# Performance work log

Measured on AMD Instinct MI355X. Metric: run time of the kernel, lower is better.

The kernel has to match this reference:

```python
import jax, jax.numpy as jnp
import numpy as np

INPUT_SIZE = 1000
EMB = 1024          # 2**ceil(log2(input_size))
NQ = 10             # log2(EMB)
NL = 3              # n_qlayers (hardcoded in module)
B = 4096


def _rot(phi, theta, omega):
    # PennyLane qml.Rot(phi, theta, omega) = RZ(omega) RY(theta) RZ(phi)
    c = jnp.cos(theta * 0.5).astype(jnp.complex64)
    s = jnp.sin(theta * 0.5).astype(jnp.complex64)
    ea = jnp.exp(-0.5j * (phi + omega))   # e^{-i(phi+omega)/2}
    eb = jnp.exp(0.5j * (phi - omega))    # e^{ i(phi-omega)/2}
    row0 = jnp.stack([ea * c, -eb * s])
    row1 = jnp.stack([jnp.conj(eb) * s, jnp.conj(ea) * c])
    return jnp.stack([row0, row1])        # [2, 2] complex64


def _apply_1q(psi, U, q):
    # psi: [B] + [2]*NQ ; contract qubit axis q+1 with U
    psi = jnp.tensordot(psi, U, axes=[[q + 1], [1]])
    return jnp.moveaxis(psi, -1, q + 1)


def _apply_cnot(psi, c, t):
    c_ax, t_ax = c + 1, t + 1
    psi0 = jax.lax.index_in_dim(psi, 0, axis=c_ax, keepdims=False)
    psi1 = jax.lax.index_in_dim(psi, 1, axis=c_ax, keepdims=False)
    f_ax = t_ax - 1 if t_ax > c_ax else t_ax
    psi1 = jnp.flip(psi1, axis=f_ax)      # X on target when control=1
    return jnp.stack([psi0, psi1], axis=c_ax)


def _circuit(x, w):
    # AmplitudeEmbedding(normalize=True) + StronglyEntanglingLayers + probs
    norm = jnp.sqrt(jnp.sum(x * x, axis=1, keepdims=True))
    psi = (x / norm).astype(jnp.complex64)
    b = psi.shape[0]
    psi = psi.reshape((b,) + (2,) * NQ)   # wire 0 = most-significant bit
    for l in range(NL):
        for q in range(NQ):
            psi = _apply_1q(psi, _rot(w[l, q, 0], w[l, q, 1], w[l, q, 2]), q)
        r = l % (NQ - 1) + 1              # default SEL ranges
        for q in range(NQ):
            psi = _apply_cnot(psi, q, (q + r) % NQ)
    return (psi.real ** 2 + psi.imag ** 2).reshape(b, -1)  # probs [B, 2**NQ]


def setup_inputs() -> dict:
    key = jax.random.key(0)
    ks = jax.random.split(key, 12)
    d = {
        'inputs': jax.random.normal(ks[0], (B, INPUT_SIZE), jnp.float32),
        'weightsEnc': 0.1 * jax.random.normal(ks[1], (NL, NQ, 3), jnp.float32),
        'weightsDec': 0.1 * jax.random.normal(ks[2], (NL, NQ, 3), jnp.float32),
        'W0': jax.random.normal(ks[3], (INPUT_SIZE, EMB), jnp.float32) / np.sqrt(INPUT_SIZE),
        'b0': jnp.zeros((EMB,), jnp.float32),
        'W1': jax.random.normal(ks[4], (EMB, 2 * EMB), jnp.float32) / np.sqrt(EMB),
        'b1': jnp.zeros((2 * EMB,), jnp.float32),
        'W2': jax.random.normal(ks[5], (2 * EMB, EMB), jnp.float32) / np.sqrt(2 * EMB),
        'b2': jnp.zeros((EMB,), jnp.float32),
        'W3': jax.random.normal(ks[6], (EMB, INPUT_SIZE), jnp.float32) / np.sqrt(EMB),
        'b3': jnp.zeros((INPUT_SIZE,), jnp.float32),
    }
    return d


def reference(inputs, weightsEnc, weightsDec, W0, b0, W1, b1, W2, b2, W3, b3):
    x = inputs @ W0 + b0                 # Dense(embedding_dim)
    x = _circuit(x, weightsEnc)          # encoder qnode (vmapped over batch)
    x = x @ W1 + b1                      # Dense(2*embedding_dim)
    x = x @ W2 + b2                      # Dense(embedding_dim)
    x = _circuit(x, weightsDec)          # decoder qnode
    x = x @ W3 + b3                      # Dense(input_size)
    x = jnp.abs(x)
    return x / jnp.sum(x, axis=1, keepdims=True)
```

## Files before the change

kernel.cpp:

```cpp
#include <hip/hip_runtime.h>
#include <math.h>


#define B_SZ 4096
#define EMB 1024
#define NQ 10
#define NL 3

typedef __bf16 bf16x8 __attribute__((ext_vector_type(8)));
typedef float f32x4 __attribute__((ext_vector_type(4)));
typedef unsigned short u16x8 __attribute__((ext_vector_type(8)));

__device__ __forceinline__ unsigned short f2bf_rne(float f) {
    unsigned int u = __float_as_uint(f);
    u += 0x7FFFu + ((u >> 16) & 1u);
    return (unsigned short)(u >> 16);
}
__device__ __forceinline__ float bf2f(unsigned short h) {
    return __uint_as_float(((unsigned int)h) << 16);
}
__device__ __forceinline__ float lane_bcast(float v, int l) {
    return __uint_as_float(__builtin_amdgcn_readlane(__float_as_uint(v), l));
}

template<int M>
__device__ __forceinline__ float lane_xor(float v) {
    if constexpr (M == 1)
        return __uint_as_float(__builtin_amdgcn_mov_dpp(__float_as_uint(v), 0xB1, 0xF, 0xF, true));
    else if constexpr (M == 2)
        return __uint_as_float(__builtin_amdgcn_mov_dpp(__float_as_uint(v), 0x4E, 0xF, 0xF, true));
    else if constexpr (M == 8)
        return __uint_as_float(__builtin_amdgcn_mov_dpp(__float_as_uint(v), 0x128, 0xF, 0xF, true));
    else if constexpr (M == 4)
        return __uint_as_float(__builtin_amdgcn_ds_swizzle(__float_as_uint(v), 0x101F));
    else if constexpr (M == 16)
        return __uint_as_float(__builtin_amdgcn_ds_swizzle(__float_as_uint(v), 0x401F));
    else
        return __shfl_xor(v, 32, 64);
}

__device__ __forceinline__ void gll16(const void* g, void* l) {
    __builtin_amdgcn_global_load_lds(
        (const __attribute__((address_space(1))) void*)g,
        (__attribute__((address_space(3))) void*)l, 16, 0, 0);
}

#define GBM 128
#define GBN 128
#define GBK 32

__global__ __launch_bounds__(512) void gemm3_mfma(
    const unsigned short* __restrict__ Ah, const unsigned short* __restrict__ Al,
    const unsigned short* __restrict__ Bh, const unsigned short* __restrict__ Bl,
    const float* __restrict__ bias, float* __restrict__ C,
    int Kp, int Np, int Ksplit, size_t zStride)
{
    __shared__ __align__(16) char lds[32768];
    char* ldsAh = lds;
    char* ldsAl = lds + 8192;
    char* ldsBh = lds + 16384;
    char* ldsBl = lds + 24576;

    const int tid = threadIdx.x;
    const int lane = tid & 63;
    const int wv = tid >> 6;
    const int wm = wv >> 1;
    const int wn = wv & 1;
    const int blockRow = blockIdx.y * GBM;
    const int blockCol = blockIdx.x * GBN;
    const int z = blockIdx.z;

    const int srow = tid >> 2;
    const int skel = (tid & 3) * 8;
    const size_t aOff = ((size_t)(blockRow + srow) * Kp + skel + (size_t)z * Ksplit) * 2;
    const size_t bOff = ((size_t)(blockCol + srow) * Kp + skel + (size_t)z * Ksplit) * 2;
    const char* aHp = (const char*)Ah + aOff;
    const char* aLp = (const char*)Al + aOff;
    const char* bHp = (const char*)Bh + bOff;
    const char* bLp = (const char*)Bl + bOff;
    const int stageOff = wv * 1024;

    f32x4 acc[2][4];
    #pragma unroll
    for (int i = 0; i < 2; ++i)
        #pragma unroll
        for (int j = 0; j < 4; ++j)
            #pragma unroll
            for (int r = 0; r < 4; ++r) acc[i][j][r] = 0.f;

    const int kq = (lane >> 4) * 16;
    int aFragOff[2], bFragOff[4];
    #pragma unroll
    for (int i = 0; i < 2; ++i) aFragOff[i] = (wm * 32 + i * 16 + (lane & 15)) * 64 + kq;
    #pragma unroll
    for (int j = 0; j < 4; ++j) bFragOff[j] = (wn * 64 + j * 16 + (lane & 15)) * 64 + kq;

    const int nsteps = Ksplit / GBK;
    for (int s = 0; s < nsteps; ++s) {
        const size_t kb = (size_t)s * GBK * 2;
        gll16(aHp + kb, ldsAh + stageOff);
        gll16(aLp + kb, ldsAl + stageOff);
        gll16(bHp + kb, ldsBh + stageOff);
        gll16(bLp + kb, ldsBl + stageOff);
        __syncthreads();

        bf16x8 ah[2], al[2], bh[4], bl[4];
        #pragma unroll
        for (int i = 0; i < 2; ++i) {
            ah[i] = *(const bf16x8*)(ldsAh + aFragOff[i]);
            al[i] = *(const bf16x8*)(ldsAl + aFragOff[i]);
        }
        #pragma unroll
        for (int j = 0; j < 4; ++j) {
            bh[j] = *(const bf16x8*)(ldsBh + bFragOff[j]);
            bl[j] = *(const bf16x8*)(ldsBl + bFragOff[j]);
        }
        #pragma unroll
        for (int j = 0; j < 4; ++j)
            #pragma unroll
            for (int i = 0; i < 2; ++i) {
                acc[i][j] = __builtin_amdgcn_mfma_f32_16x16x32_bf16(al[i], bh[j], acc[i][j], 0, 0, 0);
                acc[i][j] = __builtin_amdgcn_mfma_f32_16x16x32_bf16(ah[i], bl[j], acc[i][j], 0, 0, 0);
                acc[i][j] = __builtin_amdgcn_mfma_f32_16x16x32_bf16(ah[i], bh[j], acc[i][j], 0, 0, 0);
            }
        __syncthreads();
    }

    float* Cz = C + (size_t)z * zStride;
    const bool addB = (z == 0) && (bias != nullptr);
    const int rquad = (lane >> 4) * 4;
    const int cidx = lane & 15;
    #pragma unroll
    for (int i = 0; i < 2; ++i)
        #pragma unroll
        for (int j = 0; j < 4; ++j) {
            #pragma unroll
            for (int r = 0; r < 4; ++r) {
                int row = blockRow + wm * 32 + i * 16 + rquad + r;
                int col = blockCol + wn * 64 + j * 16 + cidx;
                float v = acc[i][j][r];
                if (addB) v += bias[col];
                Cz[(size_t)row * Np + col] = v;
            }
        }
}

__device__ __forceinline__ void tsplit_block(
    const float* __restrict__ W, unsigned short* __restrict__ H, unsigned short* __restrict__ L,
    int K, int N, int Kp, int bx, int by, int tid)
{
    __shared__ float tile[32][33];
    const int tx = tid & 31, ty = tid >> 5;
    const int k0 = bx * 32, n0 = by * 32;
    #pragma unroll
    for (int i = 0; i < 4; ++i) {
        int k = k0 + ty + i * 8, n = n0 + tx;
        tile[ty + i * 8][tx] = (k < K && n < N) ? W[(size_t)k * N + n] : 0.f;
    }
    __syncthreads();
    #pragma unroll
    for (int i = 0; i < 4; ++i) {
        int n = n0 + ty + i * 8, k = k0 + tx;
        float v = tile[tx][ty + i * 8];
        size_t o = (size_t)n * Kp + k;
        unsigned short h = f2bf_rne(v);
        H[o] = h;
        L[o] = f2bf_rne(v - bf2f(h));
    }
}

__global__ __launch_bounds__(256) void prep_weights_kernel(
    const float* __restrict__ W0, unsigned short* __restrict__ Bt0h, unsigned short* __restrict__ Bt0l,
    const float* __restrict__ W2, unsigned short* __restrict__ Bt2h, unsigned short* __restrict__ Bt2l,
    const float* __restrict__ W3, unsigned short* __restrict__ Bt3h, unsigned short* __restrict__ Bt3l,
    const float* __restrict__ W1, unsigned short* __restrict__ W1h, unsigned short* __restrict__ W1l)
{
    const int bid = blockIdx.x;
    const int tid = threadIdx.x;
    if (bid < 1024) {
        tsplit_block(W0, Bt0h, Bt0l, 1000, 1024, 1024, bid & 31, bid >> 5, tid);
    } else if (bid < 3072) {
        int b = bid - 1024;
        tsplit_block(W2, Bt2h, Bt2l, 2048, 1024, 2048, b & 63, b >> 6, tid);
    } else if (bid < 4096) {
        int b = bid - 3072;
        tsplit_block(W3, Bt3h, Bt3l, 1024, 1000, 1024, b & 31, b >> 5, tid);
    } else {
        int r = bid - 4096;
        for (int c = tid; c < 2048; c += 256) {
            float v = W1[(size_t)r * 2048 + c];
            unsigned short h = f2bf_rne(v);
            size_t o = (size_t)r * 2048 + c;
            W1h[o] = h;
            W1l[o] = f2bf_rne(v - bf2f(h));
        }
    }
}

__global__ __launch_bounds__(256) void prep_misc_kernel(
    const float* __restrict__ b1, const float* __restrict__ W2, const float* __restrict__ b2,
    float* __restrict__ b12,
    const float* __restrict__ b3, float* __restrict__ b3p,
    const float* __restrict__ wEnc, const float* __restrict__ wDec, float* __restrict__ G)
{
    __shared__ float red[4][64];
    const int bid = blockIdx.x;
    const int tid = threadIdx.x;
    if (bid < 16) {
        const int tx = tid & 63, ty = tid >> 6;
        const int n = bid * 64 + tx;
        float s = 0.f;
        for (int j = ty * 512; j < (ty + 1) * 512; ++j)
            s += b1[j] * W2[(size_t)j * 1024 + n];
        red[ty][tx] = s;
        __syncthreads();
        if (ty == 0) b12[n] = red[0][tx] + red[1][tx] + red[2][tx] + red[3][tx] + b2[n];
    } else if (bid < 20) {
        int i = (bid - 16) * 256 + tid;
        b3p[i] = (i < 1000) ? b3[i] : 0.f;
    } else {
        int g = tid;
        if (g < 60) {
            const float* w = (g < 30) ? (wEnc + g * 3) : (wDec + (g - 30) * 3);
            float* o = G + ((g < 30) ? g : (g - 30 + 64)) * 8;
            float phi = w[0], th = w[1], om = w[2];
            float ch = cosf(0.5f * th), sh = sinf(0.5f * th);
            float ap = 0.5f * (phi + om), am = 0.5f * (phi - om);
            float cap = cosf(ap), sap = sinf(ap);
            float cam = cosf(am), sam = sinf(am);
            o[0] =  cap * ch; o[1] = -sap * ch;
            o[2] = -cam * sh; o[3] = -sam * sh;
            o[4] =  cam * sh; o[5] = -sam * sh;
            o[6] =  cap * ch; o[7] =  sap * ch;
        }
    }
}

__global__ __launch_bounds__(256) void tsplit8_kernel(
    const float* __restrict__ P, unsigned short* __restrict__ H, unsigned short* __restrict__ L)
{
    __shared__ float tile[32][33];
    const int tid = threadIdx.x;
    const int tx = tid & 31, ty = tid >> 5;
    const int k0 = blockIdx.x * 32, n0 = blockIdx.y * 32;
    #pragma unroll
    for (int i = 0; i < 4; ++i) {
        int k = k0 + ty + i * 8, n = n0 + tx;
        size_t o = (size_t)k * 1024 + n;
        float s = 0.f;
        #pragma unroll
        for (int zz = 0; zz < 8; ++zz) s += P[o + ((size_t)zz << 20)];
        tile[ty + i * 8][tx] = s;
    }
    __syncthreads();
    #pragma unroll
    for (int i = 0; i < 4; ++i) {
        int n = n0 + ty + i * 8, k = k0 + tx;
        float v = tile[tx][ty + i * 8];
        size_t o = (size_t)n * 1024 + k;
        unsigned short h = f2bf_rne(v);
        H[o] = h;
        L[o] = f2bf_rne(v - bf2f(h));
    }
}

__global__ __launch_bounds__(256) void split_rows_kernel(
    const float* __restrict__ X, unsigned short* __restrict__ H, unsigned short* __restrict__ L,
    int C, int Cp)
{
    const int r = blockIdx.x;
    for (int c = threadIdx.x; c < Cp; c += 256) {
        float v = (c < C) ? X[(size_t)r * C + c] : 0.f;
        unsigned short h = f2bf_rne(v);
        size_t o = (size_t)r * Cp + c;
        H[o] = h;
        L[o] = f2bf_rne(v - bf2f(h));
    }
}


template<int GATE, int Q>
__device__ __forceinline__ void apply_rot(float (&xr)[16], float (&xi)[16],
                                          const float (&tbl)[8], int lane)
{
    float are = lane_bcast(tbl[0], GATE), aim = lane_bcast(tbl[1], GATE);
    float bre = lane_bcast(tbl[2], GATE), bim = lane_bcast(tbl[3], GATE);
    float cre = lane_bcast(tbl[4], GATE), cim = lane_bcast(tbl[5], GATE);
    float dre = lane_bcast(tbl[6], GATE), dim_ = lane_bcast(tbl[7], GATE);
    constexpr int S = 1 << (9 - Q);
    if constexpr (S < 16) {
        #pragma unroll
        for (int p = 0; p < 8; ++p) {
            int r0 = (p / S) * (2 * S) + (p % S);
            int r1 = r0 + S;
            float x0r = xr[r0], x0i = xi[r0], x1r = xr[r1], x1i = xi[r1];
            xr[r0] = are * x0r - aim * x0i + bre * x1r - bim * x1i;
            xi[r0] = are * x0i + aim * x0r + bre * x1i + bim * x1r;
            xr[r1] = cre * x0r - cim * x0i + dre * x1r - dim_ * x1i;
            xi[r1] = cre * x0i + cim * x0r + dre * x1i + dim_ * x1r;
        }
    } else {
        constexpr int M = S >> 4;
        bool bit = (lane & M) != 0;
        float pre = bit ? dre : are, pim = bit ? dim_ : aim;
        float qre = bit ? cre : bre, qim = bit ? cim : bim;
        #pragma unroll
        for (int r = 0; r < 16; ++r) {
            float ore = lane_xor<M>(xr[r]);
            float oim = lane_xor<M>(xi[r]);
            float nr = pre * xr[r] - pim * xi[r] + qre * ore - qim * oim;
            float ni = pre * xi[r] + pim * xr[r] + qre * oim + qim * ore;
            xr[r] = nr; xi[r] = ni;
        }
    }
}

template<int C, int T>
__device__ __forceinline__ void apply_cnot(float (&xr)[16], float (&xi)[16], int lane)
{
    constexpr int SC = 1 << (9 - C), ST = 1 << (9 - T);
    if constexpr (SC < 16 && ST < 16) {
        #pragma unroll
        for (int r = 0; r < 16; ++r) {
            if ((r & SC) && !(r & ST)) {
                int j = r | ST;
                float t;
                t = xr[r]; xr[r] = xr[j]; xr[j] = t;
                t = xi[r]; xi[r] = xi[j]; xi[j] = t;
            }
        }
    } else if constexpr (SC < 16) {
        constexpr int MT = ST >> 4;
        #pragma unroll
        for (int r = 0; r < 16; ++r) {
            if (r & SC) {
                xr[r] = lane_xor<MT>(xr[r]);
                xi[r] = lane_xor<MT>(xi[r]);
            }
        }
    } else if constexpr (ST < 16) {
        constexpr int MC = SC >> 4;
        bool bit = (lane & MC) != 0;
        #pragma unroll
        for (int r = 0; r < 16; ++r) {
            if (!(r & ST)) {
                int j = r | ST;
                float a0 = xr[r], a1 = xr[j];
                xr[r] = bit ? a1 : a0;  xr[j] = bit ? a0 : a1;
                float b0 = xi[r], b1 = xi[j];
                xi[r] = bit ? b1 : b0;  xi[j] = bit ? b0 : b1;
            }
        }
    } else {
        constexpr int MC = SC >> 4, MT = ST >> 4;
        bool bit = (lane & MC) != 0;
        #pragma unroll
        for (int r = 0; r < 16; ++r) {
            float o = lane_xor<MT>(xr[r]);
            xr[r] = bit ? o : xr[r];
            float oi = lane_xor<MT>(xi[r]);
            xi[r] = bit ? oi : xi[r];
        }
    }
}

template<int L, int Q>
__device__ __forceinline__ void rots(float (&xr)[16], float (&xi)[16],
                                     const float (&tbl)[8], int lane) {
    apply_rot<L * 10 + Q, Q>(xr, xi, tbl, lane);
    if constexpr (Q < 9) rots<L, Q + 1>(xr, xi, tbl, lane);
}
template<int L, int Q>
__device__ __forceinline__ void cnots(float (&xr)[16], float (&xi)[16], int lane) {
    constexpr int R = (L % 9) + 1;
    apply_cnot<Q, (Q + R) % 10>(xr, xi, lane);
    if constexpr (Q < 9) cnots<L, Q + 1>(xr, xi, lane);
}

__global__ __launch_bounds__(256, 4) void circuit_reg_kernel(
    const float* __restrict__ X0, const float* __restrict__ X1,
    unsigned short* __restrict__ Ph, unsigned short* __restrict__ Pl,
    const float* __restrict__ G)
{
    const int lane = threadIdx.x & 63;
    const int item = blockIdx.x * 4 + (threadIdx.x >> 6);
    const size_t base = (size_t)item * 1024 + lane * 16;

    float tbl[8];
    {
        const float4* gp = (const float4*)(G + lane * 8);
        float4 t0 = gp[0], t1 = gp[1];
        tbl[0] = t0.x; tbl[1] = t0.y; tbl[2] = t0.z; tbl[3] = t0.w;
        tbl[4] = t1.x; tbl[5] = t1.y; tbl[6] = t1.z; tbl[7] = t1.w;
    }

    float xr[16], xi[16];
    const float4* xb0 = (const float4*)(X0 + base);
    const float4* xb1 = (const float4*)(X1 + base);
    #pragma unroll
    for (int v = 0; v < 4; ++v) {
        float4 f = xb0[v], g = xb1[v];
        xr[v * 4 + 0] = f.x + g.x; xr[v * 4 + 1] = f.y + g.y;
        xr[v * 4 + 2] = f.z + g.z; xr[v * 4 + 3] = f.w + g.w;
    }
    #pragma unroll
    for (int r = 0; r < 16; ++r) xi[r] = 0.f;

    float nrm = 0.f;
    #pragma unroll
    for (int r = 0; r < 16; ++r) nrm += xr[r] * xr[r];
    nrm += lane_xor<1>(nrm);
    nrm += lane_xor<2>(nrm);
    nrm += lane_xor<4>(nrm);
    nrm += lane_xor<8>(nrm);
    nrm += lane_xor<16>(nrm);
    nrm += lane_xor<32>(nrm);
    float inv = 1.0f / sqrtf(nrm);
    #pragma unroll
    for (int r = 0; r < 16; ++r) xr[r] *= inv;

    rots<0, 0>(xr, xi, tbl, lane);  cnots<0, 0>(xr, xi, lane);
    rots<1, 0>(xr, xi, tbl, lane);  cnots<1, 0>(xr, xi, lane);
    rots<2, 0>(xr, xi, tbl, lane);  cnots<2, 0>(xr, xi, lane);

    u16x8 h[2], lo[2];
    #pragma unroll
    for (int r = 0; r < 16; ++r) {
        float p = xr[r] * xr[r] + xi[r] * xi[r];
        unsigned short hh = f2bf_rne(p);
        h[r >> 3][r & 7] = hh;
        lo[r >> 3][r & 7] = f2bf_rne(p - bf2f(hh));
    }
    *(u16x8*)(Ph + base) = h[0];
    *(u16x8*)(Ph + base + 8) = h[1];
    *(u16x8*)(Pl + base) = lo[0];
    *(u16x8*)(Pl + base + 8) = lo[1];
}

__global__ __launch_bounds__(256) void absnorm_kernel(
    const float* __restrict__ X0, const float* __restrict__ X1,
    float* __restrict__ out, int N, int stride)
{
    __shared__ float red[4];
    const int row = blockIdx.x;
    const int tid = threadIdx.x;
    const float* x0 = X0 + (size_t)row * stride;
    const float* x1 = X1 + (size_t)row * stride;

    float s = 0.f;
    for (int i = tid; i < N; i += 256) s += fabsf(x0[i] + x1[i]);
    #pragma unroll
    for (int off = 32; off > 0; off >>= 1) s += __shfl_down(s, off);
    if ((tid & 63) == 0) red[tid >> 6] = s;
    __syncthreads();
    float inv = 1.0f / (red[0] + red[1] + red[2] + red[3]);
    for (int i = tid; i < N; i += 256)
        out[(size_t)row * N + i] = fabsf(x0[i] + x1[i]) * inv;
}

extern "C" void kernel_launch(void* const* d_in, const int* in_sizes, int n_in,
                              void* d_out, int out_size, void* d_ws, size_t ws_size,
                              hipStream_t stream)
{
    const float* inputs = (const float*)d_in[0];
    const float* wEnc   = (const float*)d_in[1];
    const float* wDec   = (const float*)d_in[2];
    const float* W0     = (const float*)d_in[3];
    const float* b0     = (const float*)d_in[4];
    const float* W1     = (const float*)d_in[5];
    const float* b1     = (const float*)d_in[6];
    const float* W2     = (const float*)d_in[7];
    const float* b2     = (const float*)d_in[8];
    const float* W3     = (const float*)d_in[9];
    const float* b3     = (const float*)d_in[10];
    float* out = (float*)d_out;

    char* w = (char*)d_ws;
    auto alloc = [&](size_t bytes) { char* p = w; w += (bytes + 255) & ~(size_t)255; return p; };

    unsigned short* Bt0h  = (unsigned short*)alloc((size_t)1024 * 1024 * 2);
    unsigned short* Bt0l  = (unsigned short*)alloc((size_t)1024 * 1024 * 2);
    unsigned short* Bt2h  = (unsigned short*)alloc((size_t)1024 * 2048 * 2);
    unsigned short* Bt2l  = (unsigned short*)alloc((size_t)1024 * 2048 * 2);
    unsigned short* Bt3h  = (unsigned short*)alloc((size_t)1024 * 1024 * 2);
    unsigned short* Bt3l  = (unsigned short*)alloc((size_t)1024 * 1024 * 2);
    unsigned short* Bt12h = (unsigned short*)alloc((size_t)1024 * 1024 * 2);
    unsigned short* Bt12l = (unsigned short*)alloc((size_t)1024 * 1024 * 2);
    unsigned short* W1h   = (unsigned short*)alloc((size_t)1024 * 2048 * 2);
    unsigned short* W1l   = (unsigned short*)alloc((size_t)1024 * 2048 * 2);
    float*          b3p   = (float*)alloc(1024 * 4);
    float*          b12   = (float*)alloc(1024 * 4);
    float*          G     = (float*)alloc(2 * 512 * 4);
    unsigned short* Ah    = (unsigned short*)alloc((size_t)B_SZ * 1024 * 2);
    unsigned short* Al    = (unsigned short*)alloc((size_t)B_SZ * 1024 * 2);
    unsigned short* ph    = (unsigned short*)alloc((size_t)B_SZ * 1024 * 2);
    unsigned short* pl    = (unsigned short*)alloc((size_t)B_SZ * 1024 * 2);
    float*          P     = (float*)alloc((size_t)2 * B_SZ * 1024 * 4);
    float* P12 = P;
    const size_t ZS = (size_t)B_SZ * 1024;

    dim3 blk256(256);

    prep_weights_kernel<<<5120, blk256, 0, stream>>>(
        W0, Bt0h, Bt0l, W2, Bt2h, Bt2l, W3, Bt3h, Bt3l, W1, W1h, W1l);
    prep_misc_kernel<<<21, blk256, 0, stream>>>(b1, W2, b2, b12, b3, b3p, wEnc, wDec, G);
    split_rows_kernel<<<B_SZ, blk256, 0, stream>>>(inputs, Ah, Al, 1000, 1024);

    gemm3_mfma<<<dim3(8, 8, 8), 512, 0, stream>>>(
        W1h, W1l, Bt2h, Bt2l, nullptr, P12, 2048, 1024, 256, (size_t)1 << 20);
    tsplit8_kernel<<<dim3(32, 32), blk256, 0, stream>>>(P12, Bt12h, Bt12l);

    gemm3_mfma<<<dim3(8, 32, 2), 512, 0, stream>>>(
        Ah, Al, Bt0h, Bt0l, b0, P, 1024, 1024, 512, ZS);
    circuit_reg_kernel<<<B_SZ / 4, blk256, 0, stream>>>(P, P + ZS, ph, pl, G);
    gemm3_mfma<<<dim3(8, 32, 2), 512, 0, stream>>>(
        ph, pl, Bt12h, Bt12l, b12, P, 1024, 1024, 512, ZS);
    circuit_reg_kernel<<<B_SZ / 4, blk256, 0, stream>>>(P, P + ZS, ph, pl, G + 512);
    gemm3_mfma<<<dim3(8, 32, 2), 512, 0, stream>>>(
        ph, pl, Bt3h, Bt3l, b3p, P, 1024, 1024, 512, ZS);
    absnorm_kernel<<<B_SZ, blk256, 0, stream>>>(P, P + ZS, out, 1000, 1024);
}
```

Baseline: 413.4 us.

## Raise split-K to four slices, two items per wave in circuit, merge prep kernels

The three main GEMMs now use split-K of 4 (K chunk 256) instead of 2, which doubles the grid to fill more CUs. The circuit and absnorm kernels are updated to sum four partial slices. Each circuit wave now simulates two batch items (32 amplitudes per lane) with fewer waves per SM, amortising gate-parameter broadcasts and adding ILP. The prep, misc and input-split kernels are merged into a single launch. The cost is twice the partial-sum traffic and memory, plus higher register pressure in the circuit kernel.

```diff
diff --git a/kernel.cpp b/kernel.cpp
--- a/kernel.cpp
+++ b/kernel.cpp
@@ -169,11 +169,15 @@
     }
 }
 
-__global__ __launch_bounds__(256) void prep_weights_kernel(
+__global__ __launch_bounds__(256) void prep_all_kernel(
     const float* __restrict__ W0, unsigned short* __restrict__ Bt0h, unsigned short* __restrict__ Bt0l,
     const float* __restrict__ W2, unsigned short* __restrict__ Bt2h, unsigned short* __restrict__ Bt2l,
     const float* __restrict__ W3, unsigned short* __restrict__ Bt3h, unsigned short* __restrict__ Bt3l,
-    const float* __restrict__ W1, unsigned short* __restrict__ W1h, unsigned short* __restrict__ W1l)
+    const float* __restrict__ W1, unsigned short* __restrict__ W1h, unsigned short* __restrict__ W1l,
+    const float* __restrict__ X, unsigned short* __restrict__ Ah, unsigned short* __restrict__ Al,
+    const float* __restrict__ b1, const float* __restrict__ b2, float* __restrict__ b12,
+    const float* __restrict__ b3, float* __restrict__ b3p,
+    const float* __restrict__ wEnc, const float* __restrict__ wDec, float* __restrict__ G)
 {
     const int bid = blockIdx.x;
     const int tid = threadIdx.x;
@@ -185,7 +189,7 @@
     } else if (bid < 4096) {
         int b = bid - 3072;
         tsplit_block(W3, Bt3h, Bt3l, 1024, 1000, 1024, b & 31, b >> 5, tid);
-    } else {
+    } else if (bid < 5120) {
         int r = bid - 4096;
         for (int c = tid; c < 2048; c += 256) {
             float v = W1[(size_t)r * 2048 + c];
@@ -194,29 +198,27 @@
             W1h[o] = h;
             W1l[o] = f2bf_rne(v - bf2f(h));
         }
-    }
-}
-
-__global__ __launch_bounds__(256) void prep_misc_kernel(
-    const float* __restrict__ b1, const float* __restrict__ W2, const float* __restrict__ b2,
-    float* __restrict__ b12,
-    const float* __restrict__ b3, float* __restrict__ b3p,
-    const float* __restrict__ wEnc, const float* __restrict__ wDec, float* __restrict__ G)
-{
-    __shared__ float red[4][64];
-    const int bid = blockIdx.x;
-    const int tid = threadIdx.x;
-    if (bid < 16) {
+    } else if (bid < 9216) {
+        int r = bid - 5120;
+        for (int c = tid; c < 1024; c += 256) {
+            float v = (c < 1000) ? X[(size_t)r * 1000 + c] : 0.f;
+            unsigned short h = f2bf_rne(v);
+            size_t o = (size_t)r * 1024 + c;
+            Ah[o] = h;
+            Al[o] = f2bf_rne(v - bf2f(h));
+        }
+    } else if (bid < 9232) {
+        __shared__ float red[4][64];
         const int tx = tid & 63, ty = tid >> 6;
-        const int n = bid * 64 + tx;
+        const int n = (bid - 9216) * 64 + tx;
         float s = 0.f;
         for (int j = ty * 512; j < (ty + 1) * 512; ++j)
             s += b1[j] * W2[(size_t)j * 1024 + n];
         red[ty][tx] = s;
         __syncthreads();
         if (ty == 0) b12[n] = red[0][tx] + red[1][tx] + red[2][tx] + red[3][tx] + b2[n];
-    } else if (bid < 20) {
-        int i = (bid - 16) * 256 + tid;
+    } else if (bid < 9236) {
+        int i = (bid - 9232) * 256 + tid;
         b3p[i] = (i < 1000) ? b3[i] : 0.f;
     } else {
         int g = tid;
@@ -264,23 +266,9 @@
     }
 }
 
-__global__ __launch_bounds__(256) void split_rows_kernel(
-    const float* __restrict__ X, unsigned short* __restrict__ H, unsigned short* __restrict__ L,
-    int C, int Cp)
-{
-    const int r = blockIdx.x;
-    for (int c = threadIdx.x; c < Cp; c += 256) {
-        float v = (c < C) ? X[(size_t)r * C + c] : 0.f;
-        unsigned short h = f2bf_rne(v);
-        size_t o = (size_t)r * Cp + c;
-        H[o] = h;
-        L[o] = f2bf_rne(v - bf2f(h));
-    }
-}
-
 
 template<int GATE, int Q>
-__device__ __forceinline__ void apply_rot(float (&xr)[16], float (&xi)[16],
+__device__ __forceinline__ void apply_rot(float (&xr)[32], float (&xi)[32],
                                           const float (&tbl)[8], int lane)
 {
     float are = lane_bcast(tbl[0], GATE), aim = lane_bcast(tbl[1], GATE);
@@ -290,22 +278,24 @@
     constexpr int S = 1 << (9 - Q);
     if constexpr (S < 16) {
         #pragma unroll
-        for (int p = 0; p < 8; ++p) {
-            int r0 = (p / S) * (2 * S) + (p % S);
-            int r1 = r0 + S;
-            float x0r = xr[r0], x0i = xi[r0], x1r = xr[r1], x1i = xi[r1];
-            xr[r0] = are * x0r - aim * x0i + bre * x1r - bim * x1i;
-            xi[r0] = are * x0i + aim * x0r + bre * x1i + bim * x1r;
-            xr[r1] = cre * x0r - cim * x0i + dre * x1r - dim_ * x1i;
-            xi[r1] = cre * x0i + cim * x0r + dre * x1i + dim_ * x1r;
-        }
+        for (int it = 0; it < 32; it += 16)
+            #pragma unroll
+            for (int p = 0; p < 8; ++p) {
+                int r0 = it + (p / S) * (2 * S) + (p % S);
+                int r1 = r0 + S;
+                float x0r = xr[r0], x0i = xi[r0], x1r = xr[r1], x1i = xi[r1];
+                xr[r0] = are * x0r - aim * x0i + bre * x1r - bim * x1i;
+                xi[r0] = are * x0i + aim * x0r + bre * x1i + bim * x1r;
+                xr[r1] = cre * x0r - cim * x0i + dre * x1r - dim_ * x1i;
+                xi[r1] = cre * x0i + cim * x0r + dre * x1i + dim_ * x1r;
+            }
     } else {
         constexpr int M = S >> 4;
         bool bit = (lane & M) != 0;
         float pre = bit ? dre : are, pim = bit ? dim_ : aim;
         float qre = bit ? cre : bre, qim = bit ? cim : bim;
         #pragma unroll
-        for (int r = 0; r < 16; ++r) {
+        for (int r = 0; r < 32; ++r) {
             float ore = lane_xor<M>(xr[r]);
             float oim = lane_xor<M>(xi[r]);
             float nr = pre * xr[r] - pim * xi[r] + qre * ore - qim * oim;
@@ -316,46 +306,53 @@
 }
 
 template<int C, int T>
-__device__ __forceinline__ void apply_cnot(float (&xr)[16], float (&xi)[16], int lane)
+__device__ __forceinline__ void apply_cnot(float (&xr)[32], float (&xi)[32], int lane)
 {
     constexpr int SC = 1 << (9 - C), ST = 1 << (9 - T);
     if constexpr (SC < 16 && ST < 16) {
         #pragma unroll
-        for (int r = 0; r < 16; ++r) {
-            if ((r & SC) && !(r & ST)) {
-                int j = r | ST;
-                float t;
-                t = xr[r]; xr[r] = xr[j]; xr[j] = t;
-                t = xi[r]; xi[r] = xi[j]; xi[j] = t;
+        for (int it = 0; it < 32; it += 16)
+            #pragma unroll
+            for (int r = 0; r < 16; ++r) {
+                if ((r & SC) && !(r & ST)) {
+                    int a = it + r, j = it + (r | ST);
+                    float t;
+                    t = xr[a]; xr[a] = xr[j]; xr[j] = t;
+                    t = xi[a]; xi[a] = xi[j]; xi[j] = t;
+                }
             }
-        }
     } else if constexpr (SC < 16) {
         constexpr int MT = ST >> 4;
         #pragma unroll
-        for (int r = 0; r < 16; ++r) {
-            if (r & SC) {
-                xr[r] = lane_xor<MT>(xr[r]);
-                xi[r] = lane_xor<MT>(xi[r]);
+        for (int it = 0; it < 32; it += 16)
+            #pragma unroll
+            for (int r = 0; r < 16; ++r) {
+                if (r & SC) {
+                    xr[it + r] = lane_xor<MT>(xr[it + r]);
+                    xi[it + r] = lane_xor<MT>(xi[it + r]);
+                }
             }
-        }
     } else if constexpr (ST < 16) {
         constexpr int MC = SC >> 4;
         bool bit = (lane & MC) != 0;
         #pragma unroll
-        for (int r = 0; r < 16; ++r) {
-            if (!(r & ST)) {
-                int j = r | ST;
-                float a0 = xr[r], a1 = xr[j];
-                xr[r] = bit ? a1 : a0;  xr[j] = bit ? a0 : a1;
-                float b0 = xi[r], b1 = xi[j];
-                xi[r] = bit ? b1 : b0;  xi[j] = bit ? b0 : b1;
+        for (int it = 0; it < 32; it += 16)
+            #pragma unroll
+            for (int r = 0; r < 16; ++r) {
+                if (!(r & ST)) {
+                    int a = it + r, j = it + (r | ST);
+                    float a0 = xr[a], a1 = xr[j];
+                    xr[a] = bit ? a1 : a0;  xr[j] = bit ? a0 : a1;
+                    float b0 = xi[a], b1 = xi[j];
+                    xi[a] = bit ? b1 : b0;  xi[j] = bit ? b0 : b1;
+                }
             }
-        }
     } else {
-        constexpr int MC = SC >> 4, MT = ST >> 4;
+        constexpr int MT = ST >> 4;
+        constexpr int MC = SC >> 4;
         bool bit = (lane & MC) != 0;
         #pragma unroll
-        for (int r = 0; r < 16; ++r) {
+        for (int r = 0; r < 32; ++r) {
             float o = lane_xor<MT>(xr[r]);
             xr[r] = bit ? o : xr[r];
             float oi = lane_xor<MT>(xi[r]);
@@ -365,26 +362,27 @@
 }
 
 template<int L, int Q>
-__device__ __forceinline__ void rots(float (&xr)[16], float (&xi)[16],
+__device__ __forceinline__ void rots(float (&xr)[32], float (&xi)[32],
                                      const float (&tbl)[8], int lane) {
     apply_rot<L * 10 + Q, Q>(xr, xi, tbl, lane);
     if constexpr (Q < 9) rots<L, Q + 1>(xr, xi, tbl, lane);
 }
 template<int L, int Q>
-__device__ __forceinline__ void cnots(float (&xr)[16], float (&xi)[16], int lane) {
+__device__ __forceinline__ void cnots(float (&xr)[32], float (&xi)[32], int lane) {
     constexpr int R = (L % 9) + 1;
     apply_cnot<Q, (Q + R) % 10>(xr, xi, lane);
     if constexpr (Q < 9) cnots<L, Q + 1>(xr, xi, lane);
 }
 
-__global__ __launch_bounds__(256, 4) void circuit_reg_kernel(
-    const float* __restrict__ X0, const float* __restrict__ X1,
+__global__ __launch_bounds__(256, 2) void circuit_reg_kernel(
+    const float* __restrict__ P, size_t ZS,
     unsigned short* __restrict__ Ph, unsigned short* __restrict__ Pl,
     const float* __restrict__ G)
 {
     const int lane = threadIdx.x & 63;
-    const int item = blockIdx.x * 4 + (threadIdx.x >> 6);
-    const size_t base = (size_t)item * 1024 + lane * 16;
+    const int item0 = blockIdx.x * 4 + (threadIdx.x >> 6);
+    const size_t base0 = (size_t)item0 * 1024 + lane * 16;
+    const size_t base1 = base0 + (size_t)2048 * 1024;
 
     float tbl[8];
     {
@@ -394,68 +392,89 @@
         tbl[4] = t1.x; tbl[5] = t1.y; tbl[6] = t1.z; tbl[7] = t1.w;
     }
 
-    float xr[16], xi[16];
-    const float4* xb0 = (const float4*)(X0 + base);
-    const float4* xb1 = (const float4*)(X1 + base);
-    #pragma unroll
-    for (int v = 0; v < 4; ++v) {
-        float4 f = xb0[v], g = xb1[v];
-        xr[v * 4 + 0] = f.x + g.x; xr[v * 4 + 1] = f.y + g.y;
-        xr[v * 4 + 2] = f.z + g.z; xr[v * 4 + 3] = f.w + g.w;
-    }
-    #pragma unroll
-    for (int r = 0; r < 16; ++r) xi[r] = 0.f;
-
-    float nrm = 0.f;
-    #pragma unroll
-    for (int r = 0; r < 16; ++r) nrm += xr[r] * xr[r];
-    nrm += lane_xor<1>(nrm);
-    nrm += lane_xor<2>(nrm);
-    nrm += lane_xor<4>(nrm);
-    nrm += lane_xor<8>(nrm);
-    nrm += lane_xor<16>(nrm);
-    nrm += lane_xor<32>(nrm);
-    float inv = 1.0f / sqrtf(nrm);
-    #pragma unroll
-    for (int r = 0; r < 16; ++r) xr[r] *= inv;
+    float xr[32], xi[32];
+    #pragma unroll
+    for (int it = 0; it < 2; ++it) {
+        const size_t b = it ? base1 : base0;
+        const float4* p0 = (const float4*)(P + b);
+        const float4* p1 = (const float4*)(P + ZS + b);
+        const float4* p2 = (const float4*)(P + 2 * ZS + b);
+        const float4* p3 = (const float4*)(P + 3 * ZS + b);
+        #pragma unroll
+        for (int v = 0; v < 4; ++v) {
+            float4 a = p0[v], bb = p1[v], c = p2[v], d = p3[v];
+            xr[it * 16 + v * 4 + 0] = a.x + bb.x + c.x + d.x;
+            xr[it * 16 + v * 4 + 1] = a.y + bb.y + c.y + d.y;
+            xr[it * 16 + v * 4 + 2] = a.z + bb.z + c.z + d.z;
+            xr[it * 16 + v * 4 + 3] = a.w + bb.w + c.w + d.w;
+        }
+    }
+    #pragma unroll
+    for (int r = 0; r < 32; ++r) xi[r] = 0.f;
+
+    float n0 = 0.f, n1 = 0.f;
+    #pragma unroll
+    for (int r = 0; r < 16; ++r) { n0 += xr[r] * xr[r]; n1 += xr[16 + r] * xr[16 + r]; }
+    n0 += lane_xor<1>(n0);   n1 += lane_xor<1>(n1);
+    n0 += lane_xor<2>(n0);   n1 += lane_xor<2>(n1);
+    n0 += lane_xor<4>(n0);   n1 += lane_xor<4>(n1);
+    n0 += lane_xor<8>(n0);   n1 += lane_xor<8>(n1);
+    n0 += lane_xor<16>(n0);  n1 += lane_xor<16>(n1);
+    n0 += lane_xor<32>(n0);  n1 += lane_xor<32>(n1);
+    float inv0 = 1.0f / sqrtf(n0), inv1 = 1.0f / sqrtf(n1);
+    #pragma unroll
+    for (int r = 0; r < 16; ++r) { xr[r] *= inv0; xr[16 + r] *= inv1; }
 
     rots<0, 0>(xr, xi, tbl, lane);  cnots<0, 0>(xr, xi, lane);
     rots<1, 0>(xr, xi, tbl, lane);  cnots<1, 0>(xr, xi, lane);
     rots<2, 0>(xr, xi, tbl, lane);  cnots<2, 0>(xr, xi, lane);
 
-    u16x8 h[2], lo[2];
-    #pragma unroll
-    for (int r = 0; r < 16; ++r) {
-        float p = xr[r] * xr[r] + xi[r] * xi[r];
-        unsigned short hh = f2bf_rne(p);
-        h[r >> 3][r & 7] = hh;
-        lo[r >> 3][r & 7] = f2bf_rne(p - bf2f(hh));
-    }
-    *(u16x8*)(Ph + base) = h[0];
-    *(u16x8*)(Ph + base + 8) = h[1];
-    *(u16x8*)(Pl + base) = lo[0];
-    *(u16x8*)(Pl + base + 8) = lo[1];
+    #pragma unroll
+    for (int it = 0; it < 2; ++it) {
+        const size_t b = it ? base1 : base0;
+        u16x8 h[2], lo[2];
+        #pragma unroll
+        for (int r = 0; r < 16; ++r) {
+            float pr = xr[it * 16 + r], pi = xi[it * 16 + r];
+            float p = pr * pr + pi * pi;
+            unsigned short hh = f2bf_rne(p);
+            h[r >> 3][r & 7] = hh;
+            lo[r >> 3][r & 7] = f2bf_rne(p - bf2f(hh));
+        }
+        *(u16x8*)(Ph + b) = h[0];
+        *(u16x8*)(Ph + b + 8) = h[1];
+        *(u16x8*)(Pl + b) = lo[0];
+        *(u16x8*)(Pl + b + 8) = lo[1];
+    }
 }
 
 __global__ __launch_bounds__(256) void absnorm_kernel(
-    const float* __restrict__ X0, const float* __restrict__ X1,
-    float* __restrict__ out, int N, int stride)
+    const float* __restrict__ P, size_t ZS, float* __restrict__ out, int N)
 {
     __shared__ float red[4];
     const int row = blockIdx.x;
     const int tid = threadIdx.x;
-    const float* x0 = X0 + (size_t)row * stride;
-    const float* x1 = X1 + (size_t)row * stride;
-
+    const size_t rb = (size_t)row * 1024 + tid * 4;
+
+    float4 a = *(const float4*)(P + rb);
+    float4 b = *(const float4*)(P + ZS + rb);
+    float4 c = *(const float4*)(P + 2 * ZS + rb);
+    float4 d = *(const float4*)(P + 3 * ZS + rb);
+    float x[4] = { a.x + b.x + c.x + d.x, a.y + b.y + c.y + d.y,
+                   a.z + b.z + c.z + d.z, a.w + b.w + c.w + d.w };
+
+    const int c0 = tid * 4;
     float s = 0.f;
-    for (int i = tid; i < N; i += 256) s += fabsf(x0[i] + x1[i]);
+    #pragma unroll
+    for (int j = 0; j < 4; ++j) if (c0 + j < N) s += fabsf(x[j]);
     #pragma unroll
     for (int off = 32; off > 0; off >>= 1) s += __shfl_down(s, off);
     if ((tid & 63) == 0) red[tid >> 6] = s;
     __syncthreads();
     float inv = 1.0f / (red[0] + red[1] + red[2] + red[3]);
-    for (int i = tid; i < N; i += 256)
-        out[(size_t)row * N + i] = fabsf(x0[i] + x1[i]) * inv;
+    #pragma unroll
+    for (int j = 0; j < 4; ++j)
+        if (c0 + j < N) out[(size_t)row * N + c0 + j] = fabsf(x[j]) * inv;
 }
 
 extern "C" void kernel_launch(void* const* d_in, const int* in_sizes, int n_in,
@@ -495,28 +514,27 @@
     unsigned short* Al    = (unsigned short*)alloc((size_t)B_SZ * 1024 * 2);
     unsigned short* ph    = (unsigned short*)alloc((size_t)B_SZ * 1024 * 2);
     unsigned short* pl    = (unsigned short*)alloc((size_t)B_SZ * 1024 * 2);
-    float*          P     = (float*)alloc((size_t)2 * B_SZ * 1024 * 4);
+    float*          P     = (float*)alloc((size_t)4 * B_SZ * 1024 * 4);
     float* P12 = P;
     const size_t ZS = (size_t)B_SZ * 1024;
 
     dim3 blk256(256);
 
-    prep_weights_kernel<<<5120, blk256, 0, stream>>>(
-        W0, Bt0h, Bt0l, W2, Bt2h, Bt2l, W3, Bt3h, Bt3l, W1, W1h, W1l);
-    prep_misc_kernel<<<21, blk256, 0, stream>>>(b1, W2, b2, b12, b3, b3p, wEnc, wDec, G);
-    split_rows_kernel<<<B_SZ, blk256, 0, stream>>>(inputs, Ah, Al, 1000, 1024);
+    prep_all_kernel<<<9237, blk256, 0, stream>>>(
+        W0, Bt0h, Bt0l, W2, Bt2h, Bt2l, W3, Bt3h, Bt3l, W1, W1h, W1l,
+        inputs, Ah, Al, b1, b2, b12, b3, b3p, wEnc, wDec, G);
 
     gemm3_mfma<<<dim3(8, 8, 8), 512, 0, stream>>>(
         W1h, W1l, Bt2h, Bt2l, nullptr, P12, 2048, 1024, 256, (size_t)1 << 20);
     tsplit8_kernel<<<dim3(32, 32), blk256, 0, stream>>>(P12, Bt12h, Bt12l);
 
-    gemm3_mfma<<<dim3(8, 32, 2), 512, 0, stream>>>(
-        Ah, Al, Bt0h, Bt0l, b0, P, 1024, 1024, 512, ZS);
-    circuit_reg_kernel<<<B_SZ / 4, blk256, 0, stream>>>(P, P + ZS, ph, pl, G);
-    gemm3_mfma<<<dim3(8, 32, 2), 512, 0, stream>>>(
-        ph, pl, Bt12h, Bt12l, b12, P, 1024, 1024, 512, ZS);
-    circuit_reg_kernel<<<B_SZ / 4, blk256, 0, stream>>>(P, P + ZS, ph, pl, G + 512);
-    gemm3_mfma<<<dim3(8, 32, 2), 512, 0, stream>>>(
-        ph, pl, Bt3h, Bt3l, b3p, P, 1024, 1024, 512, ZS);
-    absnorm_kernel<<<B_SZ, blk256, 0, stream>>>(P, P + ZS, out, 1000, 1024);
-}
+    gemm3_mfma<<<dim3(8, 32, 4), 512, 0, stream>>>(
+        Ah, Al, Bt0h, Bt0l, b0, P, 1024, 1024, 256, ZS);
+    circuit_reg_kernel<<<512, blk256, 0, stream>>>(P, ZS, ph, pl, G);
+    gemm3_mfma<<<dim3(8, 32, 4), 512, 0, stream>>>(
+        ph, pl, Bt12h, Bt12l, b12, P, 1024, 1024, 256, ZS);
+    circuit_reg_kernel<<<512, blk256, 0, stream>>>(P, ZS, ph, pl, G + 512);
+    gemm3_mfma<<<dim3(8, 32, 4), 512, 0, stream>>>(
+        ph, pl, Bt3h, Bt3l, b3p, P, 1024, 1024, 256, ZS);
+    absnorm_kernel<<<B_SZ, blk256, 0, stream>>>(P, ZS, out, 1000);
+}
```

New measurement: 439.5 us. 1.06x slower.
